# Optimization experiments

Measured on AMD Instinct MI355X. Metric: run time of the kernel, lower is better.

Reference implementation:

```python
import jax, jax.numpy as jnp
import numpy as np

N, CX, CS, H = 2048, 768, 384, 16
D = CX // H  # 48


def _ln(t, eps=1e-5):
    mu = jnp.mean(t, axis=-1, keepdims=True)
    var = jnp.mean(jnp.square(t - mu), axis=-1, keepdims=True)
    return (t - mu) * jax.lax.rsqrt(var + eps)


def setup_inputs() -> dict:
    key = jax.random.key(0)
    ks = jax.random.split(key, 16)
    s = 0.02
    return {
        "x": jax.random.normal(ks[0], (N, CX), jnp.float32),
        "mask": jax.random.randint(ks[1], (N,), 0, 2, jnp.int32),
        "pair_logits": jax.random.normal(ks[2], (H, N, N), jnp.float32),
        "single_cond": jax.random.normal(ks[3], (N, CS), jnp.float32),
        # AdaptiveLayerNorm params (single_cond LN has weight, no bias)
        "ln_sc_w": jnp.ones((CS,), jnp.float32),
        "sc_scale_w": s * jax.random.normal(ks[4], (CS, CX), jnp.float32),
        "sc_scale_b": jnp.zeros((CX,), jnp.float32),
        "sc_bias_w": s * jax.random.normal(ks[5], (CS, CX), jnp.float32),
        # q/k/v/gating projections (stored as (in, out); y = x @ W)
        "q_w": s * jax.random.normal(ks[6], (CX, CX), jnp.float32),
        "q_b": jnp.zeros((CX,), jnp.float32),
        "k_w": s * jax.random.normal(ks[7], (CX, CX), jnp.float32),
        "v_w": s * jax.random.normal(ks[8], (CX, CX), jnp.float32),
        "gate_w": s * jax.random.normal(ks[9], (CX, CX), jnp.float32),
        # AdaLNZero params
        "out_w": s * jax.random.normal(ks[10], (CX, CX), jnp.float32),
        "azc_w": s * jax.random.normal(ks[11], (CS, CX), jnp.float32),
        "azc_b": jnp.zeros((CX,), jnp.float32),
    }


def reference(x, mask, pair_logits, single_cond, ln_sc_w, sc_scale_w, sc_scale_b,
              sc_bias_w, q_w, q_b, k_w, v_w, gate_w, out_w, azc_w, azc_b):
    # AdaptiveLayerNorm (use_single_cond=True)
    xn = _ln(x)                              # (N, CX), no affine
    sc = _ln(single_cond) * ln_sc_w          # (N, CS), weight only
    xa = jax.nn.sigmoid(sc @ sc_scale_w + sc_scale_b) * xn + sc @ sc_bias_w

    # QKV projections, split into heads: (N, H, D)
    q = (xa @ q_w + q_b).reshape(N, H, D)
    k = (xa @ k_w).reshape(N, H, D)
    v = (xa @ v_w).reshape(N, H, D)

    # Attention with per-head additive pair bias and key mask
    logits = jnp.einsum("qhd,khd->hqk", q * (D ** -0.5), k) + pair_logits
    logits = jnp.where(mask.astype(bool)[None, None, :], logits, -1e9)
    w = jax.nn.softmax(logits, axis=-1)      # (H, N, N)
    wa = jnp.einsum("hqk,khd->qhd", w, v).reshape(N, CX)

    # Gating, then AdaLNZero output
    wa = wa * jax.nn.sigmoid(xa @ gate_w)
    out = (wa @ out_w) * jax.nn.sigmoid(sc @ azc_w + azc_b)
    return out
```

## Files before the change

### kernel.cpp

```cpp
#include <hip/hip_runtime.h>
#include <math.h>

#define NN 2048
#define CXX 768
#define CSS 384
#define HH 16
#define DHH 48

typedef short bf16x8 __attribute__((ext_vector_type(8)));
typedef float f32x4 __attribute__((ext_vector_type(4)));

#define MFMA16(a,b,c) __builtin_amdgcn_mfma_f32_16x16x32_bf16(a,b,c,0,0,0)

__device__ __forceinline__ unsigned short f2bf(float f){
  unsigned u = __float_as_uint(f);
  u += 0x7FFFu + ((u >> 16) & 1u);
  return (unsigned short)(u >> 16);
}
__device__ __forceinline__ float bf2f(unsigned short u){
  return __uint_as_float(((unsigned)u) << 16);
}
__device__ __forceinline__ void async_copy16(const void* g, void* l){
  __builtin_amdgcn_global_load_lds((const __attribute__((address_space(1))) void*)g,
                                   (__attribute__((address_space(3))) void*)l, 16, 0, 0);
}

__device__ inline float waveReduceSum(float v){
  #pragma unroll
  for(int o=32;o>0;o>>=1) v += __shfl_xor(v,o);
  return v;
}

__global__ __launch_bounds__(256) void transpose_all(
    const float* __restrict__ s0, const float* __restrict__ s1, const float* __restrict__ s2,
    const float* __restrict__ s3, const float* __restrict__ s4, const float* __restrict__ s5,
    const float* __restrict__ s6, const float* __restrict__ s7,
    unsigned short* __restrict__ d_scale, unsigned short* __restrict__ d_bias,
    unsigned short* __restrict__ d_azc, unsigned short* __restrict__ d_qkvg,
    unsigned short* __restrict__ d_out){
  int z = blockIdx.z;
  const float* W; unsigned short* Wt; int K;
  switch(z){
    case 0: W=s0; Wt=d_scale; K=384; break;
    case 1: W=s1; Wt=d_bias;  K=384; break;
    case 2: W=s2; Wt=d_azc;   K=384; break;
    case 3: W=s3; Wt=d_qkvg + 0*589824; K=768; break;
    case 4: W=s4; Wt=d_qkvg + 1*589824; K=768; break;
    case 5: W=s5; Wt=d_qkvg + 2*589824; K=768; break;
    case 6: W=s6; Wt=d_qkvg + 3*589824; K=768; break;
    default: W=s7; Wt=d_out; K=768; break;
  }
  int n0 = blockIdx.x*32, k0 = blockIdx.y*32;
  if(k0 >= K) return;
  __shared__ unsigned short t[32][33];
  int c = threadIdx.x & 31, r = threadIdx.x >> 5;
  #pragma unroll
  for(int i=0;i<32;i+=8){
    float v = W[(size_t)(k0 + r + i)*CXX + n0 + c];
    t[c][r+i] = f2bf(v);
  }
  __syncthreads();
  #pragma unroll
  for(int i=0;i<32;i+=8){
    Wt[(size_t)(n0 + r + i)*K + k0 + c] = t[r+i][c];
  }
}

__global__ __launch_bounds__(384) void ln_fused(const float* __restrict__ x,
    const float* __restrict__ scin, const float* __restrict__ w,
    float* __restrict__ xn, unsigned short* __restrict__ scb){
  int row = blockIdx.x;
  int t = threadIdx.x;
  int wid = t>>6, lane = t&63;
  __shared__ float red[6];
  float a0 = x[(size_t)row*CXX + t];
  float a1 = x[(size_t)row*CXX + 384 + t];
  float s = waveReduceSum(a0+a1);
  if(lane==0) red[wid]=s;
  __syncthreads();
  float mu = (red[0]+red[1]+red[2]+red[3]+red[4]+red[5]) * (1.0f/CXX);
  float d0=a0-mu, d1=a1-mu;
  float q = waveReduceSum(d0*d0+d1*d1);
  __syncthreads();
  if(lane==0) red[wid]=q;
  __syncthreads();
  float var = (red[0]+red[1]+red[2]+red[3]+red[4]+red[5]) * (1.0f/CXX);
  float r = rsqrtf(var + 1e-5f);
  xn[(size_t)row*CXX + t] = d0*r;
  xn[(size_t)row*CXX + 384 + t] = d1*r;
  float b = scin[(size_t)row*CSS + t];
  float s2 = waveReduceSum(b);
  __syncthreads();
  if(lane==0) red[wid]=s2;
  __syncthreads();
  float mu2 = (red[0]+red[1]+red[2]+red[3]+red[4]+red[5]) * (1.0f/CSS);
  float d2 = b - mu2;
  float q2 = waveReduceSum(d2*d2);
  __syncthreads();
  if(lane==0) red[wid]=q2;
  __syncthreads();
  float var2 = (red[0]+red[1]+red[2]+red[3]+red[4]+red[5]) * (1.0f/CSS);
  float r2 = rsqrtf(var2 + 1e-5f);
  scb[(size_t)row*CSS + t] = f2bf(d2*r2*w[t]);
}

__global__ __launch_bounds__(256) void gemm_qkvg(const unsigned short* __restrict__ A,
    const unsigned short* __restrict__ Bt, const float* __restrict__ bias,
    unsigned short* __restrict__ C){
  __shared__ unsigned short As[2][128*32];
  __shared__ unsigned short Bs[2][128*32];
  const int tid = threadIdx.x;
  const int w = tid>>6, lane = tid&63;
  const int ln15 = lane&15, hi = lane>>4;
  const int wm = w&1, wn = w>>1;
  const int m0 = blockIdx.y*128, n0 = blockIdx.x*128;
  const int lrow = lane>>2, lk = (lane&3)*8;
  const int K = 768, NC = 3072;

  f32x4 z = {0.f,0.f,0.f,0.f};
  f32x4 acc[4][4];
  #pragma unroll
  for(int i=0;i<4;i++)
    #pragma unroll
    for(int j=0;j<4;j++) acc[i][j] = z;

  for(int k0=0;k0<K;k0+=64){
    const unsigned short* ga = A + (size_t)(m0 + w*32 + lrow)*K + k0 + lk;
    const unsigned short* gb = Bt + (size_t)(n0 + w*32 + lrow)*K + k0 + lk;
    async_copy16(ga,             &As[0][w*1024]);
    async_copy16(ga + 16*K,      &As[0][w*1024 + 512]);
    async_copy16(gb,             &Bs[0][w*1024]);
    async_copy16(gb + 16*K,      &Bs[0][w*1024 + 512]);
    async_copy16(ga + 32,        &As[1][w*1024]);
    async_copy16(ga + 16*K + 32, &As[1][w*1024 + 512]);
    async_copy16(gb + 32,        &Bs[1][w*1024]);
    async_copy16(gb + 16*K + 32, &Bs[1][w*1024 + 512]);
    __syncthreads();
    #pragma unroll
    for(int half=0; half<2; ++half){
      bf16x8 af[4], bfr[4];
      #pragma unroll
      for(int i=0;i<4;i++) af[i]  = *(const bf16x8*)&As[half][(wm*64 + i*16 + ln15)*32 + hi*8];
      #pragma unroll
      for(int j=0;j<4;j++) bfr[j] = *(const bf16x8*)&Bs[half][(wn*64 + j*16 + ln15)*32 + hi*8];
      #pragma unroll
      for(int i=0;i<4;i++)
        #pragma unroll
        for(int j=0;j<4;j++)
          acc[i][j] = MFMA16(af[i], bfr[j], acc[i][j]);
    }
    __syncthreads();
  }

  #pragma unroll
  for(int i=0;i<4;i++)
    #pragma unroll
    for(int j=0;j<4;j++)
      #pragma unroll
      for(int r=0;r<4;r++){
        int gm = m0 + wm*64 + i*16 + hi*4 + r;
        int gn = n0 + wn*64 + j*16 + ln15;
        float v = acc[i][j][r];
        if(gn < 768) v += bias[gn];
        if(gn >= 2304) v = 1.0f/(1.0f + __expf(-v));
        C[(size_t)gm*NC + gn] = f2bf(v);
      }
}

__global__ __launch_bounds__(256) void adaln3(const unsigned short* __restrict__ A,
    const unsigned short* __restrict__ B1, const unsigned short* __restrict__ B2,
    const unsigned short* __restrict__ B3, const float* __restrict__ bs,
    const float* __restrict__ zb, const float* __restrict__ xn,
    unsigned short* __restrict__ xa, float* __restrict__ azc){
  __shared__ unsigned short As [2][64*32];
  __shared__ unsigned short Bs1[2][64*32];
  __shared__ unsigned short Bs2[2][64*32];
  __shared__ unsigned short Bs3[2][64*32];
  const int tid = threadIdx.x;
  const int w = tid>>6, lane = tid&63;
  const int ln15 = lane&15, hi = lane>>4;
  const int wm = w&1, wn = w>>1;
  const int m0 = blockIdx.y*64, n0 = blockIdx.x*64;
  const int lrow = tid>>2, lk = (tid&3)*8;
  const int K = CSS;

  f32x4 z = {0.f,0.f,0.f,0.f};
  f32x4 acc1[2][2], acc2[2][2], acc3[2][2];
  #pragma unroll
  for(int i=0;i<2;i++)
    #pragma unroll
    for(int j=0;j<2;j++){ acc1[i][j]=z; acc2[i][j]=z; acc3[i][j]=z; }

  for(int k0=0;k0<K;k0+=64){
    const unsigned short* ga = A  + (size_t)(m0+lrow)*K + k0 + lk;
    const unsigned short* g1 = B1 + (size_t)(n0+lrow)*K + k0 + lk;
    const unsigned short* g2 = B2 + (size_t)(n0+lrow)*K + k0 + lk;
    const unsigned short* g3 = B3 + (size_t)(n0+lrow)*K + k0 + lk;
    async_copy16(ga,      &As [0][w*512]);
    async_copy16(g1,      &Bs1[0][w*512]);
    async_copy16(g2,      &Bs2[0][w*512]);
    async_copy16(g3,      &Bs3[0][w*512]);
    async_copy16(ga + 32, &As [1][w*512]);
    async_copy16(g1 + 32, &Bs1[1][w*512]);
    async_copy16(g2 + 32, &Bs2[1][w*512]);
    async_copy16(g3 + 32, &Bs3[1][w*512]);
    __syncthreads();
    #pragma unroll
    for(int half=0; half<2; ++half){
      bf16x8 af[2], b1f[2], b2f[2], b3f[2];
      #pragma unroll
      for(int i=0;i<2;i++) af[i]  = *(const bf16x8*)&As[half][(wm*32 + i*16 + ln15)*32 + hi*8];
      #pragma unroll
      for(int j=0;j<2;j++){
        b1f[j] = *(const bf16x8*)&Bs1[half][(wn*32 + j*16 + ln15)*32 + hi*8];
        b2f[j] = *(const bf16x8*)&Bs2[half][(wn*32 + j*16 + ln15)*32 + hi*8];
        b3f[j] = *(const bf16x8*)&Bs3[half][(wn*32 + j*16 + ln15)*32 + hi*8];
      }
      #pragma unroll
      for(int i=0;i<2;i++)
        #pragma unroll
        for(int j=0;j<2;j++){
          acc1[i][j] = MFMA16(af[i], b1f[j], acc1[i][j]);
          acc2[i][j] = MFMA16(af[i], b2f[j], acc2[i][j]);
          acc3[i][j] = MFMA16(af[i], b3f[j], acc3[i][j]);
        }
    }
    __syncthreads();
  }

  #pragma unroll
  for(int i=0;i<2;i++)
    #pragma unroll
    for(int j=0;j<2;j++)
      #pragma unroll
      for(int r=0;r<4;r++){
        int gm = m0 + wm*32 + i*16 + hi*4 + r;
        int gn = n0 + wn*32 + j*16 + ln15;
        float g = 1.0f/(1.0f + __expf(-(acc1[i][j][r] + bs[gn])));
        float v = g * xn[(size_t)gm*CXX + gn] + acc2[i][j][r];
        xa[(size_t)gm*CXX + gn] = f2bf(v);
        azc[(size_t)gm*CXX + gn] = 1.0f/(1.0f + __expf(-(acc3[i][j][r] + zb[gn])));
      }
}

__global__ __launch_bounds__(256) void gemm_out(const unsigned short* __restrict__ A,
    const unsigned short* __restrict__ Bt, const float* __restrict__ mul,
    float* __restrict__ C){
  __shared__ unsigned short As[2][64*32];
  __shared__ unsigned short Bs[2][64*32];
  const int tid = threadIdx.x;
  const int w = tid>>6, lane = tid&63;
  const int ln15 = lane&15, hi = lane>>4;
  const int wm = w&1, wn = w>>1;
  const int m0 = blockIdx.y*64, n0 = blockIdx.x*64;
  const int lrow = tid>>2, lk = (tid&3)*8;
  const int K = 768;

  f32x4 z = {0.f,0.f,0.f,0.f};
  f32x4 acc[2][2];
  #pragma unroll
  for(int i=0;i<2;i++)
    #pragma unroll
    for(int j=0;j<2;j++) acc[i][j]=z;

  for(int k0=0;k0<K;k0+=64){
    const unsigned short* ga = A  + (size_t)(m0+lrow)*K + k0 + lk;
    const unsigned short* gb = Bt + (size_t)(n0+lrow)*K + k0 + lk;
    async_copy16(ga,      &As[0][w*512]);
    async_copy16(gb,      &Bs[0][w*512]);
    async_copy16(ga + 32, &As[1][w*512]);
    async_copy16(gb + 32, &Bs[1][w*512]);
    __syncthreads();
    #pragma unroll
    for(int half=0; half<2; ++half){
      bf16x8 af[2], bfr[2];
      #pragma unroll
      for(int i=0;i<2;i++) af[i]  = *(const bf16x8*)&As[half][(wm*32 + i*16 + ln15)*32 + hi*8];
      #pragma unroll
      for(int j=0;j<2;j++) bfr[j] = *(const bf16x8*)&Bs[half][(wn*32 + j*16 + ln15)*32 + hi*8];
      #pragma unroll
      for(int i=0;i<2;i++)
        #pragma unroll
        for(int j=0;j<2;j++)
          acc[i][j] = MFMA16(af[i], bfr[j], acc[i][j]);
    }
    __syncthreads();
  }

  #pragma unroll
  for(int i=0;i<2;i++)
    #pragma unroll
    for(int j=0;j<2;j++)
      #pragma unroll
      for(int r=0;r<4;r++){
        int gm = m0 + wm*32 + i*16 + hi*4 + r;
        int gn = n0 + wn*32 + j*16 + ln15;
        C[(size_t)gm*CXX + gn] = acc[i][j][r] * mul[(size_t)gm*CXX + gn];
      }
}

__global__ __launch_bounds__(256) void attn_mfma(const unsigned short* __restrict__ qkvg,
    const float* __restrict__ pair, const int* __restrict__ mask,
    unsigned short* __restrict__ wag){
  const int h = blockIdx.y;
  const int q0 = blockIdx.x*64;
  const int tid = threadIdx.x;
  const int w = tid>>6, lane = tid&63;
  const int ln15 = lane&15, hi = lane>>4;

  __shared__ unsigned short Qs[64*72];
  __shared__ unsigned short Ks[64*72];
  __shared__ unsigned short VsT[48*72];
  __shared__ unsigned short Ps[4][16*72];

  for(int idx=tid; idx<64*16; idx+=256){
    int row = idx>>4, d = 48 + (idx&15);
    Qs[row*72 + d] = 0;
    Ks[row*72 + d] = 0;
  }
  for(int idx=tid; idx<64*12; idx+=256){
    int qr = idx&63, d0 = (idx>>6)*4;
    ushort4 v = *(const ushort4*)&qkvg[(size_t)(q0+qr)*3072 + h*DHH + d0];
    *(ushort4*)&Qs[qr*72 + d0] = v;
  }
  __syncthreads();

  bf16x8 aq0 = *(const bf16x8*)&Qs[(w*16+ln15)*72 + hi*8];
  bf16x8 aq1 = *(const bf16x8*)&Qs[(w*16+ln15)*72 + 32 + hi*8];

  f32x4 z = {0.f,0.f,0.f,0.f};
  f32x4 oacc[3] = {z,z,z};
  float mold[4] = {-1e30f,-1e30f,-1e30f,-1e30f};
  float l[4] = {0.f,0.f,0.f,0.f};
  const float scale = 0.14433756729740643f;
  const int qrb = w*16 + hi*4;

  ushort4 kreg[3], vreg[3];
  int mreg[4];
  float preg[4][4];
  {
    #pragma unroll
    for(int it=0;it<3;it++){
      int idx = tid + it*256;
      int key = idx&63, d0 = (idx>>6)*4;
      kreg[it] = *(const ushort4*)&qkvg[(size_t)key*3072 +  768 + h*DHH + d0];
      vreg[it] = *(const ushort4*)&qkvg[(size_t)key*3072 + 1536 + h*DHH + d0];
    }
    #pragma unroll
    for(int jt=0;jt<4;jt++) mreg[jt] = mask[jt*16 + ln15];
    const float* pb = pair + ((size_t)h*NN + (size_t)(q0+qrb))*NN + ln15;
    #pragma unroll
    for(int r=0;r<4;r++)
      #pragma unroll
      for(int jt=0;jt<4;jt++)
        preg[jt][r] = pb[(size_t)r*NN + jt*16];
  }

  for(int kt=0; kt<NN/64; ++kt){
    __syncthreads();
    #pragma unroll
    for(int it=0;it<3;it++){
      int idx = tid + it*256;
      int key = idx&63, d0 = (idx>>6)*4;
      ushort4 kv = kreg[it];
      *(ushort4*)&Ks[key*72 + d0] = kv;
      ushort4 vv = vreg[it];
      VsT[(d0+0)*72 + key] = vv.x;
      VsT[(d0+1)*72 + key] = vv.y;
      VsT[(d0+2)*72 + key] = vv.z;
      VsT[(d0+3)*72 + key] = vv.w;
    }
    __syncthreads();

    float pc[4][4]; int mc[4];
    #pragma unroll
    for(int jt=0;jt<4;jt++){
      mc[jt] = mreg[jt];
      #pragma unroll
      for(int r=0;r<4;r++) pc[jt][r] = preg[jt][r];
    }
    {
      int k0n = (kt < NN/64 - 1) ? (kt+1)*64 : 0;
      #pragma unroll
      for(int it=0;it<3;it++){
        int idx = tid + it*256;
        int key = idx&63, d0 = (idx>>6)*4;
        kreg[it] = *(const ushort4*)&qkvg[(size_t)(k0n+key)*3072 +  768 + h*DHH + d0];
        vreg[it] = *(const ushort4*)&qkvg[(size_t)(k0n+key)*3072 + 1536 + h*DHH + d0];
      }
      #pragma unroll
      for(int jt=0;jt<4;jt++) mreg[jt] = mask[k0n + jt*16 + ln15];
      const float* pb = pair + ((size_t)h*NN + (size_t)(q0+qrb))*NN + k0n + ln15;
      #pragma unroll
      for(int r=0;r<4;r++)
        #pragma unroll
        for(int jt=0;jt<4;jt++)
          preg[jt][r] = pb[(size_t)r*NN + jt*16];
    }

    f32x4 sreg[4];
    __builtin_amdgcn_s_setprio(1);
    #pragma unroll
    for(int jt=0;jt<4;jt++){
      bf16x8 bk0 = *(const bf16x8*)&Ks[(jt*16+ln15)*72 + hi*8];
      bf16x8 bk1 = *(const bf16x8*)&Ks[(jt*16+ln15)*72 + 32 + hi*8];
      f32x4 s = z;
      s = MFMA16(aq0, bk0, s);
      s = MFMA16(aq1, bk1, s);
      sreg[jt] = s;
    }
    __builtin_amdgcn_s_setprio(0);

    float sv[4][4];
    #pragma unroll
    for(int jt=0;jt<4;jt++)
      #pragma unroll
      for(int r=0;r<4;r++)
        sv[jt][r] = mc[jt] ? sreg[jt][r]*scale + pc[jt][r] : -1e9f;

    float mr[4], al[4], rs[4];
    #pragma unroll
    for(int r=0;r<4;r++)
      mr[r] = fmaxf(fmaxf(sv[0][r],sv[1][r]), fmaxf(sv[2][r],sv[3][r]));
    #pragma unroll
    for(int o=1;o<16;o<<=1)
      #pragma unroll
      for(int r=0;r<4;r++) mr[r] = fmaxf(mr[r], __shfl_xor(mr[r],o));
    #pragma unroll
    for(int r=0;r<4;r++){
      float mn = fmaxf(mold[r], mr[r]);
      al[r] = __expf(mold[r] - mn);
      mold[r] = mn;
    }
    float pv[4][4];
    #pragma unroll
    for(int jt=0;jt<4;jt++)
      #pragma unroll
      for(int r=0;r<4;r++)
        pv[jt][r] = __expf(sv[jt][r] - mold[r]);
    #pragma unroll
    for(int r=0;r<4;r++) rs[r] = pv[0][r]+pv[1][r]+pv[2][r]+pv[3][r];
    #pragma unroll
    for(int o=1;o<16;o<<=1)
      #pragma unroll
      for(int r=0;r<4;r++) rs[r] += __shfl_xor(rs[r],o);
    #pragma unroll
    for(int r=0;r<4;r++) l[r] = l[r]*al[r] + rs[r];

    #pragma unroll
    for(int jt=0;jt<4;jt++)
      #pragma unroll
      for(int r=0;r<4;r++)
        Ps[w][(hi*4+r)*72 + jt*16 + ln15] = f2bf(pv[jt][r]);
    __asm__ volatile("s_waitcnt lgkmcnt(0)" ::: "memory");

    #pragma unroll
    for(int dt=0;dt<3;dt++)
      #pragma unroll
      for(int r=0;r<4;r++) oacc[dt][r] *= al[r];

    bf16x8 ap0 = *(const bf16x8*)&Ps[w][ln15*72 + hi*8];
    bf16x8 ap1 = *(const bf16x8*)&Ps[w][ln15*72 + 32 + hi*8];
    __builtin_amdgcn_s_setprio(1);
    #pragma unroll
    for(int dt=0;dt<3;dt++){
      bf16x8 bv0 = *(const bf16x8*)&VsT[(dt*16+ln15)*72 + hi*8];
      bf16x8 bv1 = *(const bf16x8*)&VsT[(dt*16+ln15)*72 + 32 + hi*8];
      oacc[dt] = MFMA16(ap0, bv0, oacc[dt]);
      oacc[dt] = MFMA16(ap1, bv1, oacc[dt]);
    }
    __builtin_amdgcn_s_setprio(0);
  }

  #pragma unroll
  for(int r=0;r<4;r++){
    float linv = 1.0f / l[r];
    int qrow = q0 + qrb + r;
    #pragma unroll
    for(int dt=0;dt<3;dt++){
      int col = h*DHH + dt*16 + ln15;
      float g = bf2f(qkvg[(size_t)qrow*3072 + 2304 + col]);
      float o = oacc[dt][r] * linv * g;
      wag[(size_t)qrow*CXX + col] = f2bf(o);
    }
  }
}

extern "C" void kernel_launch(void* const* d_in, const int* in_sizes, int n_in,
                              void* d_out, int out_size, void* d_ws, size_t ws_size,
                              hipStream_t stream) {
  const float* x           = (const float*)d_in[0];
  const int*   mask        = (const int*)  d_in[1];
  const float* pair        = (const float*)d_in[2];
  const float* single_cond = (const float*)d_in[3];
  const float* ln_sc_w     = (const float*)d_in[4];
  const float* sc_scale_w  = (const float*)d_in[5];
  const float* sc_scale_b  = (const float*)d_in[6];
  const float* sc_bias_w   = (const float*)d_in[7];
  const float* q_w         = (const float*)d_in[8];
  const float* q_b         = (const float*)d_in[9];
  const float* k_w         = (const float*)d_in[10];
  const float* v_w         = (const float*)d_in[11];
  const float* gate_w      = (const float*)d_in[12];
  const float* out_w       = (const float*)d_in[13];
  const float* azc_w       = (const float*)d_in[14];
  const float* azc_b       = (const float*)d_in[15];
  float* out = (float*)d_out;

  unsigned short* p = (unsigned short*)d_ws;
  unsigned short* Wt_scale = p;  p += 768*384;
  unsigned short* Wt_bias  = p;  p += 768*384;
  unsigned short* Wt_azc   = p;  p += 768*384;
  unsigned short* Wt_out   = p;  p += 768*768;
  unsigned short* Wt_qkvg  = p;  p += (size_t)3072*768;
  unsigned short* scb      = p;  p += 2048*384;
  unsigned short* xa       = p;  p += 2048*768;
  unsigned short* qkvg     = p;  p += (size_t)2048*3072;
  unsigned short* wag      = p;  p += 2048*768;
  float* fp = (float*)p;
  float* xn  = fp; fp += (size_t)2048*768;
  float* azc = fp;

  transpose_all<<<dim3(24,24,8), 256, 0, stream>>>(
      sc_scale_w, sc_bias_w, azc_w, q_w, k_w, v_w, gate_w, out_w,
      Wt_scale, Wt_bias, Wt_azc, Wt_qkvg, Wt_out);

  ln_fused<<<NN, 384, 0, stream>>>(x, single_cond, ln_sc_w, xn, scb);

  adaln3<<<dim3(12,32), 256, 0, stream>>>(scb, Wt_scale, Wt_bias, Wt_azc,
                                          sc_scale_b, azc_b, xn, xa, azc);

  gemm_qkvg<<<dim3(24,16), 256, 0, stream>>>(xa, Wt_qkvg, q_b, qkvg);

  attn_mfma<<<dim3(32,16), 256, 0, stream>>>(qkvg, pair, mask, wag);

  gemm_out<<<dim3(12,32), 256, 0, stream>>>(wag, Wt_out, azc, out);
}
```

Measured before the change: 571.8 us.

## Split attention over key dimension with combine kernel; shrink GEMM K-tiles to 32

The attention kernel now splits the key range in two along a third grid dimension, writing unnormalized partial outputs, row maxima and row sums to workspace. A new combine kernel merges them with log-sum-exp rescaling and applies the gate. The aim is to double the attention block count (512 to 1024) for better occupancy across the CUs, at the cost of extra fp32 partial-result traffic and one more launch. The GEMM kernels also move from 64-wide K steps to 32-wide ones with single-buffered LDS, which shrinks shared memory but doubles the number of barriers. The Q tile buffer is reused for the per-wave P tiles, which also cuts LDS in attention.

```diff
diff --git a/kernel.cpp b/kernel.cpp
--- a/kernel.cpp
+++ b/kernel.cpp
@@ -6,6 +6,7 @@
 #define CSS 384
 #define HH 16
 #define DHH 48
+#define KSPLIT 2
 
 typedef short bf16x8 __attribute__((ext_vector_type(8)));
 typedef float f32x4 __attribute__((ext_vector_type(4)));
@@ -107,8 +108,8 @@
 __global__ __launch_bounds__(256) void gemm_qkvg(const unsigned short* __restrict__ A,
     const unsigned short* __restrict__ Bt, const float* __restrict__ bias,
     unsigned short* __restrict__ C){
-  __shared__ unsigned short As[2][128*32];
-  __shared__ unsigned short Bs[2][128*32];
+  __shared__ unsigned short As[128*32];
+  __shared__ unsigned short Bs[128*32];
   const int tid = threadIdx.x;
   const int w = tid>>6, lane = tid&63;
   const int ln15 = lane&15, hi = lane>>4;
@@ -124,31 +125,24 @@
     #pragma unroll
     for(int j=0;j<4;j++) acc[i][j] = z;
 
-  for(int k0=0;k0<K;k0+=64){
+  for(int k0=0;k0<K;k0+=32){
     const unsigned short* ga = A + (size_t)(m0 + w*32 + lrow)*K + k0 + lk;
     const unsigned short* gb = Bt + (size_t)(n0 + w*32 + lrow)*K + k0 + lk;
-    async_copy16(ga,             &As[0][w*1024]);
-    async_copy16(ga + 16*K,      &As[0][w*1024 + 512]);
-    async_copy16(gb,             &Bs[0][w*1024]);
-    async_copy16(gb + 16*K,      &Bs[0][w*1024 + 512]);
-    async_copy16(ga + 32,        &As[1][w*1024]);
-    async_copy16(ga + 16*K + 32, &As[1][w*1024 + 512]);
-    async_copy16(gb + 32,        &Bs[1][w*1024]);
-    async_copy16(gb + 16*K + 32, &Bs[1][w*1024 + 512]);
-    __syncthreads();
-    #pragma unroll
-    for(int half=0; half<2; ++half){
-      bf16x8 af[4], bfr[4];
-      #pragma unroll
-      for(int i=0;i<4;i++) af[i]  = *(const bf16x8*)&As[half][(wm*64 + i*16 + ln15)*32 + hi*8];
-      #pragma unroll
-      for(int j=0;j<4;j++) bfr[j] = *(const bf16x8*)&Bs[half][(wn*64 + j*16 + ln15)*32 + hi*8];
-      #pragma unroll
-      for(int i=0;i<4;i++)
-        #pragma unroll
-        for(int j=0;j<4;j++)
-          acc[i][j] = MFMA16(af[i], bfr[j], acc[i][j]);
-    }
+    async_copy16(ga,          &As[w*1024]);
+    async_copy16(ga + 16*K,   &As[w*1024 + 512]);
+    async_copy16(gb,          &Bs[w*1024]);
+    async_copy16(gb + 16*K,   &Bs[w*1024 + 512]);
+    __syncthreads();
+    bf16x8 af[4], bfr[4];
+    #pragma unroll
+    for(int i=0;i<4;i++) af[i]  = *(const bf16x8*)&As[(wm*64 + i*16 + ln15)*32 + hi*8];
+    #pragma unroll
+    for(int j=0;j<4;j++) bfr[j] = *(const bf16x8*)&Bs[(wn*64 + j*16 + ln15)*32 + hi*8];
+    #pragma unroll
+    for(int i=0;i<4;i++)
+      #pragma unroll
+      for(int j=0;j<4;j++)
+        acc[i][j] = MFMA16(af[i], bfr[j], acc[i][j]);
     __syncthreads();
   }
 
@@ -172,10 +166,10 @@
     const unsigned short* __restrict__ B3, const float* __restrict__ bs,
     const float* __restrict__ zb, const float* __restrict__ xn,
     unsigned short* __restrict__ xa, float* __restrict__ azc){
-  __shared__ unsigned short As [2][64*32];
-  __shared__ unsigned short Bs1[2][64*32];
-  __shared__ unsigned short Bs2[2][64*32];
-  __shared__ unsigned short Bs3[2][64*32];
+  __shared__ unsigned short As[64*32];
+  __shared__ unsigned short Bs1[64*32];
+  __shared__ unsigned short Bs2[64*32];
+  __shared__ unsigned short Bs3[64*32];
   const int tid = threadIdx.x;
   const int w = tid>>6, lane = tid&63;
   const int ln15 = lane&15, hi = lane>>4;
@@ -191,40 +185,29 @@
     #pragma unroll
     for(int j=0;j<2;j++){ acc1[i][j]=z; acc2[i][j]=z; acc3[i][j]=z; }
 
-  for(int k0=0;k0<K;k0+=64){
-    const unsigned short* ga = A  + (size_t)(m0+lrow)*K + k0 + lk;
-    const unsigned short* g1 = B1 + (size_t)(n0+lrow)*K + k0 + lk;
-    const unsigned short* g2 = B2 + (size_t)(n0+lrow)*K + k0 + lk;
-    const unsigned short* g3 = B3 + (size_t)(n0+lrow)*K + k0 + lk;
-    async_copy16(ga,      &As [0][w*512]);
-    async_copy16(g1,      &Bs1[0][w*512]);
-    async_copy16(g2,      &Bs2[0][w*512]);
-    async_copy16(g3,      &Bs3[0][w*512]);
-    async_copy16(ga + 32, &As [1][w*512]);
-    async_copy16(g1 + 32, &Bs1[1][w*512]);
-    async_copy16(g2 + 32, &Bs2[1][w*512]);
-    async_copy16(g3 + 32, &Bs3[1][w*512]);
-    __syncthreads();
-    #pragma unroll
-    for(int half=0; half<2; ++half){
-      bf16x8 af[2], b1f[2], b2f[2], b3f[2];
-      #pragma unroll
-      for(int i=0;i<2;i++) af[i]  = *(const bf16x8*)&As[half][(wm*32 + i*16 + ln15)*32 + hi*8];
+  for(int k0=0;k0<K;k0+=32){
+    async_copy16(A  + (size_t)(m0+lrow)*K + k0 + lk, &As [w*512]);
+    async_copy16(B1 + (size_t)(n0+lrow)*K + k0 + lk, &Bs1[w*512]);
+    async_copy16(B2 + (size_t)(n0+lrow)*K + k0 + lk, &Bs2[w*512]);
+    async_copy16(B3 + (size_t)(n0+lrow)*K + k0 + lk, &Bs3[w*512]);
+    __syncthreads();
+    bf16x8 af[2], b1f[2], b2f[2], b3f[2];
+    #pragma unroll
+    for(int i=0;i<2;i++) af[i]  = *(const bf16x8*)&As[(wm*32 + i*16 + ln15)*32 + hi*8];
+    #pragma unroll
+    for(int j=0;j<2;j++){
+      b1f[j] = *(const bf16x8*)&Bs1[(wn*32 + j*16 + ln15)*32 + hi*8];
+      b2f[j] = *(const bf16x8*)&Bs2[(wn*32 + j*16 + ln15)*32 + hi*8];
+      b3f[j] = *(const bf16x8*)&Bs3[(wn*32 + j*16 + ln15)*32 + hi*8];
+    }
+    #pragma unroll
+    for(int i=0;i<2;i++)
       #pragma unroll
       for(int j=0;j<2;j++){
-        b1f[j] = *(const bf16x8*)&Bs1[half][(wn*32 + j*16 + ln15)*32 + hi*8];
-        b2f[j] = *(const bf16x8*)&Bs2[half][(wn*32 + j*16 + ln15)*32 + hi*8];
-        b3f[j] = *(const bf16x8*)&Bs3[half][(wn*32 + j*16 + ln15)*32 + hi*8];
+        acc1[i][j] = MFMA16(af[i], b1f[j], acc1[i][j]);
+        acc2[i][j] = MFMA16(af[i], b2f[j], acc2[i][j]);
+        acc3[i][j] = MFMA16(af[i], b3f[j], acc3[i][j]);
       }
-      #pragma unroll
-      for(int i=0;i<2;i++)
-        #pragma unroll
-        for(int j=0;j<2;j++){
-          acc1[i][j] = MFMA16(af[i], b1f[j], acc1[i][j]);
-          acc2[i][j] = MFMA16(af[i], b2f[j], acc2[i][j]);
-          acc3[i][j] = MFMA16(af[i], b3f[j], acc3[i][j]);
-        }
-    }
     __syncthreads();
   }
 
@@ -246,8 +229,8 @@
 __global__ __launch_bounds__(256) void gemm_out(const unsigned short* __restrict__ A,
     const unsigned short* __restrict__ Bt, const float* __restrict__ mul,
     float* __restrict__ C){
-  __shared__ unsigned short As[2][64*32];
-  __shared__ unsigned short Bs[2][64*32];
+  __shared__ unsigned short As[64*32];
+  __shared__ unsigned short Bs[64*32];
   const int tid = threadIdx.x;
   const int w = tid>>6, lane = tid&63;
   const int ln15 = lane&15, hi = lane>>4;
@@ -263,27 +246,20 @@
     #pragma unroll
     for(int j=0;j<2;j++) acc[i][j]=z;
 
-  for(int k0=0;k0<K;k0+=64){
-    const unsigned short* ga = A  + (size_t)(m0+lrow)*K + k0 + lk;
-    const unsigned short* gb = Bt + (size_t)(n0+lrow)*K + k0 + lk;
-    async_copy16(ga,      &As[0][w*512]);
-    async_copy16(gb,      &Bs[0][w*512]);
-    async_copy16(ga + 32, &As[1][w*512]);
-    async_copy16(gb + 32, &Bs[1][w*512]);
-    __syncthreads();
-    #pragma unroll
-    for(int half=0; half<2; ++half){
-      bf16x8 af[2], bfr[2];
-      #pragma unroll
-      for(int i=0;i<2;i++) af[i]  = *(const bf16x8*)&As[half][(wm*32 + i*16 + ln15)*32 + hi*8];
-      #pragma unroll
-      for(int j=0;j<2;j++) bfr[j] = *(const bf16x8*)&Bs[half][(wn*32 + j*16 + ln15)*32 + hi*8];
-      #pragma unroll
-      for(int i=0;i<2;i++)
-        #pragma unroll
-        for(int j=0;j<2;j++)
-          acc[i][j] = MFMA16(af[i], bfr[j], acc[i][j]);
-    }
+  for(int k0=0;k0<K;k0+=32){
+    async_copy16(A  + (size_t)(m0+lrow)*K + k0 + lk, &As[w*512]);
+    async_copy16(Bt + (size_t)(n0+lrow)*K + k0 + lk, &Bs[w*512]);
+    __syncthreads();
+    bf16x8 af[2], bfr[2];
+    #pragma unroll
+    for(int i=0;i<2;i++) af[i]  = *(const bf16x8*)&As[(wm*32 + i*16 + ln15)*32 + hi*8];
+    #pragma unroll
+    for(int j=0;j<2;j++) bfr[j] = *(const bf16x8*)&Bs[(wn*32 + j*16 + ln15)*32 + hi*8];
+    #pragma unroll
+    for(int i=0;i<2;i++)
+      #pragma unroll
+      for(int j=0;j<2;j++)
+        acc[i][j] = MFMA16(af[i], bfr[j], acc[i][j]);
     __syncthreads();
   }
 
@@ -301,32 +277,35 @@
 
 __global__ __launch_bounds__(256) void attn_mfma(const unsigned short* __restrict__ qkvg,
     const float* __restrict__ pair, const int* __restrict__ mask,
-    unsigned short* __restrict__ wag){
+    float* __restrict__ po, float* __restrict__ pm, float* __restrict__ pl){
   const int h = blockIdx.y;
   const int q0 = blockIdx.x*64;
+  const int kz = blockIdx.z;
+  const int kbase = kz*(NN/KSPLIT);
+  const int NT = (NN/KSPLIT)/64;
   const int tid = threadIdx.x;
   const int w = tid>>6, lane = tid&63;
   const int ln15 = lane&15, hi = lane>>4;
 
-  __shared__ unsigned short Qs[64*72];
+  __shared__ unsigned short QPs[64*72];
   __shared__ unsigned short Ks[64*72];
   __shared__ unsigned short VsT[48*72];
-  __shared__ unsigned short Ps[4][16*72];
 
   for(int idx=tid; idx<64*16; idx+=256){
     int row = idx>>4, d = 48 + (idx&15);
-    Qs[row*72 + d] = 0;
+    QPs[row*72 + d] = 0;
     Ks[row*72 + d] = 0;
   }
   for(int idx=tid; idx<64*12; idx+=256){
     int qr = idx&63, d0 = (idx>>6)*4;
     ushort4 v = *(const ushort4*)&qkvg[(size_t)(q0+qr)*3072 + h*DHH + d0];
-    *(ushort4*)&Qs[qr*72 + d0] = v;
-  }
-  __syncthreads();
-
-  bf16x8 aq0 = *(const bf16x8*)&Qs[(w*16+ln15)*72 + hi*8];
-  bf16x8 aq1 = *(const bf16x8*)&Qs[(w*16+ln15)*72 + 32 + hi*8];
+    *(ushort4*)&QPs[qr*72 + d0] = v;
+  }
+  __syncthreads();
+
+  bf16x8 aq0 = *(const bf16x8*)&QPs[(w*16+ln15)*72 + hi*8];
+  bf16x8 aq1 = *(const bf16x8*)&QPs[(w*16+ln15)*72 + 32 + hi*8];
+  unsigned short* Ps = &QPs[w*16*72];
 
   f32x4 z = {0.f,0.f,0.f,0.f};
   f32x4 oacc[3] = {z,z,z};
@@ -343,12 +322,12 @@
     for(int it=0;it<3;it++){
       int idx = tid + it*256;
       int key = idx&63, d0 = (idx>>6)*4;
-      kreg[it] = *(const ushort4*)&qkvg[(size_t)key*3072 +  768 + h*DHH + d0];
-      vreg[it] = *(const ushort4*)&qkvg[(size_t)key*3072 + 1536 + h*DHH + d0];
-    }
-    #pragma unroll
-    for(int jt=0;jt<4;jt++) mreg[jt] = mask[jt*16 + ln15];
-    const float* pb = pair + ((size_t)h*NN + (size_t)(q0+qrb))*NN + ln15;
+      kreg[it] = *(const ushort4*)&qkvg[(size_t)(kbase+key)*3072 +  768 + h*DHH + d0];
+      vreg[it] = *(const ushort4*)&qkvg[(size_t)(kbase+key)*3072 + 1536 + h*DHH + d0];
+    }
+    #pragma unroll
+    for(int jt=0;jt<4;jt++) mreg[jt] = mask[kbase + jt*16 + ln15];
+    const float* pb = pair + ((size_t)h*NN + (size_t)(q0+qrb))*NN + kbase + ln15;
     #pragma unroll
     for(int r=0;r<4;r++)
       #pragma unroll
@@ -356,7 +335,7 @@
         preg[jt][r] = pb[(size_t)r*NN + jt*16];
   }
 
-  for(int kt=0; kt<NN/64; ++kt){
+  for(int kt=0; kt<NT; ++kt){
     __syncthreads();
     #pragma unroll
     for(int it=0;it<3;it++){
@@ -380,7 +359,7 @@
       for(int r=0;r<4;r++) pc[jt][r] = preg[jt][r];
     }
     {
-      int k0n = (kt < NN/64 - 1) ? (kt+1)*64 : 0;
+      int k0n = (kt < NT-1) ? kbase + (kt+1)*64 : kbase;
       #pragma unroll
       for(int it=0;it<3;it++){
         int idx = tid + it*256;
@@ -451,7 +430,7 @@
     for(int jt=0;jt<4;jt++)
       #pragma unroll
       for(int r=0;r<4;r++)
-        Ps[w][(hi*4+r)*72 + jt*16 + ln15] = f2bf(pv[jt][r]);
+        Ps[(hi*4+r)*72 + jt*16 + ln15] = f2bf(pv[jt][r]);
     __asm__ volatile("s_waitcnt lgkmcnt(0)" ::: "memory");
 
     #pragma unroll
@@ -459,8 +438,8 @@
       #pragma unroll
       for(int r=0;r<4;r++) oacc[dt][r] *= al[r];
 
-    bf16x8 ap0 = *(const bf16x8*)&Ps[w][ln15*72 + hi*8];
-    bf16x8 ap1 = *(const bf16x8*)&Ps[w][ln15*72 + 32 + hi*8];
+    bf16x8 ap0 = *(const bf16x8*)&Ps[ln15*72 + hi*8];
+    bf16x8 ap1 = *(const bf16x8*)&Ps[ln15*72 + 32 + hi*8];
     __builtin_amdgcn_s_setprio(1);
     #pragma unroll
     for(int dt=0;dt<3;dt++){
@@ -474,15 +453,36 @@
 
   #pragma unroll
   for(int r=0;r<4;r++){
-    float linv = 1.0f / l[r];
     int qrow = q0 + qrb + r;
-    #pragma unroll
-    for(int dt=0;dt<3;dt++){
-      int col = h*DHH + dt*16 + ln15;
-      float g = bf2f(qkvg[(size_t)qrow*3072 + 2304 + col]);
-      float o = oacc[dt][r] * linv * g;
-      wag[(size_t)qrow*CXX + col] = f2bf(o);
-    }
+    size_t rowi = (size_t)(kz*HH + h)*NN + qrow;
+    #pragma unroll
+    for(int dt=0;dt<3;dt++)
+      po[rowi*DHH + dt*16 + ln15] = oacc[dt][r];
+    if(ln15==0){
+      pm[rowi] = mold[r];
+      pl[rowi] = l[r];
+    }
+  }
+}
+
+__global__ __launch_bounds__(256) void attn_combine(const float* __restrict__ po,
+    const float* __restrict__ pm, const float* __restrict__ pl,
+    const unsigned short* __restrict__ qkvg, unsigned short* __restrict__ wag){
+  const int row = blockIdx.x*4 + (threadIdx.x>>6);
+  const int lane = threadIdx.x & 63;
+  #pragma unroll
+  for(int i=0;i<12;i++){
+    int c = lane + i*64;
+    int hh = c / DHH, d = c - hh*DHH;
+    size_t r0 = (size_t)hh*NN + row;
+    size_t r1 = (size_t)(HH + hh)*NN + row;
+    float m0 = pm[r0], m1 = pm[r1];
+    float M = fmaxf(m0, m1);
+    float e0 = __expf(m0 - M), e1 = __expf(m1 - M);
+    float L = pl[r0]*e0 + pl[r1]*e1;
+    float v = (po[r0*DHH + d]*e0 + po[r1*DHH + d]*e1) / L;
+    float g = bf2f(qkvg[(size_t)row*3072 + 2304 + c]);
+    wag[(size_t)row*CXX + c] = f2bf(v * g);
   }
 }
 
@@ -519,7 +519,10 @@
   unsigned short* wag      = p;  p += 2048*768;
   float* fp = (float*)p;
   float* xn  = fp; fp += (size_t)2048*768;
-  float* azc = fp;
+  float* azc = fp; fp += (size_t)2048*768;
+  float* po  = fp; fp += (size_t)KSPLIT*HH*NN*DHH;
+  float* pm  = fp; fp += (size_t)KSPLIT*HH*NN;
+  float* pl  = fp;
 
   transpose_all<<<dim3(24,24,8), 256, 0, stream>>>(
       sc_scale_w, sc_bias_w, azc_w, q_w, k_w, v_w, gate_w, out_w,
@@ -532,7 +535,9 @@
 
   gemm_qkvg<<<dim3(24,16), 256, 0, stream>>>(xa, Wt_qkvg, q_b, qkvg);
 
-  attn_mfma<<<dim3(32,16), 256, 0, stream>>>(qkvg, pair, mask, wag);
+  attn_mfma<<<dim3(32,16,KSPLIT), 256, 0, stream>>>(qkvg, pair, mask, po, pm, pl);
+
+  attn_combine<<<512, 256, 0, stream>>>(po, pm, pl, qkvg, wag);
 
   gemm_out<<<dim3(12,32), 256, 0, stream>>>(wag, Wt_out, azc, out);
 }
```

Measured after the change: 556.7 us. -2.6%, faster.
